# Performance work log

Hardware: AMD Instinct MI355X
Metric: run time of the kernel (lower is better)

## Reference

```python
import jax, jax.numpy as jnp
import numpy as np

EPS = 1e-7


def _softsplat(ten_in, ten_flow):
    # Forward bilinear splatting (scatter-add), faithful to softsplat_func.
    # ten_in: [B,C,H,W], ten_flow: [B,2,H,W] (flow[:,0]=dx, flow[:,1]=dy)
    B, C, H, W = ten_in.shape
    dt = ten_in.dtype
    gx = jnp.arange(W, dtype=dt)
    gy = jnp.arange(H, dtype=dt)
    fx = gx[None, None, :] + ten_flow[:, 0]  # [B,H,W] target x
    fy = gy[None, :, None] + ten_flow[:, 1]  # [B,H,W] target y
    x0 = jnp.floor(fx)
    y0 = jnp.floor(fy)
    x0i = x0.astype(jnp.int32)
    y0i = y0.astype(jnp.int32)
    x1i = x0i + 1
    y1i = y0i + 1
    wx1 = fx - x0  # weight toward x1
    wx0 = 1.0 - wx1
    wy1 = fy - y0
    wy0 = 1.0 - wy1
    # values as [B*H*W, C] rows to scatter
    vals = jnp.transpose(ten_in, (0, 2, 3, 1)).reshape(B * H * W, C)
    boff = jnp.arange(B, dtype=jnp.int32)[:, None, None] * (H * W)  # batch offsets
    out = jnp.zeros((B * H * W, C), dtype=dt)
    corners = ((x0i, y0i, wx0 * wy0), (x1i, y0i, wx1 * wy0),
               (x0i, y1i, wx0 * wy1), (x1i, y1i, wx1 * wy1))
    for xi, yi, w in corners:
        valid = (xi >= 0) & (xi < W) & (yi >= 0) & (yi < H)
        idx = (boff + jnp.clip(yi, 0, H - 1) * W + jnp.clip(xi, 0, W - 1)).reshape(-1)
        wv = jnp.where(valid, w, jnp.zeros_like(w)).reshape(-1, 1)
        out = out.at[idx].add(vals * wv)
    return jnp.transpose(out.reshape(B, H, W, C), (0, 3, 1, 2))


def reference(ten_in, ten_flow, ten_metric):
    # warp(..., strMode='soft'): softmax-style splatting with exp(metric) weights
    m = jnp.exp(ten_metric)                       # [B,1,H,W]
    cat = jnp.concatenate([ten_in * m, m], axis=1)  # [B,C+1,H,W]
    out = _softsplat(cat, ten_flow)
    norm = out[:, -1:, :, :] + EPS                # 'addeps' default branch
    return out[:, :-1, :, :] / norm


def setup_inputs() -> dict:
    key = jax.random.key(0)
    k1, k2, k3 = jax.random.split(key, 3)
    B, C, H, W = 4, 16, 512, 960
    ten_in = jax.random.normal(k1, (B, C, H, W), dtype=jnp.float32)
    # scale flow so splatting is genuinely irregular (multi-pixel displacements)
    ten_flow = jax.random.normal(k2, (B, 2, H, W), dtype=jnp.float32) * 10.0
    ten_metric = jax.random.normal(k3, (B, 1, H, W), dtype=jnp.float32)
    return {"ten_in": ten_in, "ten_flow": ten_flow, "ten_metric": ten_metric}
```

## Files before the change

### kernel.cpp

```cpp
#include <hip/hip_runtime.h>
#include <math.h>


#define BB 4
#define CC 16
#define HH 512
#define WW 960
#define HWP (HH * WW)
#define EPSF 1e-7f

#define NSX 30
#define NSY 256
#define SPB (NSX * NSY)
#define CAPS 192

#define WS_BINS_OFF ((size_t)131072)
#define WS_INT_OFF  (WS_BINS_OFF + (size_t)BB * SPB * CAPS * 16)
#define WS_NEED6    (WS_INT_OFF + (size_t)BB * HWP * 64)

#define TSX 32
#define TSY 16
#define TNX (WW / TSX)
#define TNY (HH / TSY)
#define TPB (TNX * TNY)
#define NTILE (BB * TPB)
#define CAP 1536


__launch_bounds__(256)
__global__ void prep6(const float* __restrict__ in,
                      const float* __restrict__ flow,
                      const float* __restrict__ metric,
                      unsigned int* __restrict__ counts,
                      uint4* __restrict__ bins,
                      float4* __restrict__ inT)
{
    __shared__ unsigned int lcnt[SPB];

    int b = blockIdx.z;
    int x = blockIdx.x * 32 + (threadIdx.x & 31);
    int y = blockIdx.y * 8  + (threadIdx.x >> 5);
    int p = y * WW + x;

    unsigned int* cb = counts + (size_t)b * SPB;
    uint4*        bb = bins   + (size_t)b * SPB * CAPS;

    for (int i = threadIdx.x; i < SPB; i += 256) lcnt[i] = 0;
    __syncthreads();

    float dx = flow[(size_t)(b * 2 + 0) * HWP + p];
    float dy = flow[(size_t)(b * 2 + 1) * HWP + p];
    float m  = expf(metric[(size_t)b * HWP + p]);

    const float* ib = in + (size_t)b * CC * HWP + p;
    float4* o = inT + ((size_t)b * HWP + p) * 4;
#pragma unroll
    for (int k = 0; k < 4; ++k) {
        float4 r;
        r.x = ib[(size_t)(4 * k + 0) * HWP];
        r.y = ib[(size_t)(4 * k + 1) * HWP];
        r.z = ib[(size_t)(4 * k + 2) * HWP];
        r.w = ib[(size_t)(4 * k + 3) * HWP];
        o[k] = r;
    }

    float fx = (float)x + dx, fy = (float)y + dy;
    float x0f = floorf(fx),   y0f = floorf(fy);
    int   x0 = (int)x0f,      y0 = (int)y0f;
    float wx1 = fx - x0f,     wy1 = fy - y0f;
    float wy0m = (1.0f - wy1) * m, wy1m = wy1 * m;

    int sxA = x0 >> 5, sxB = (x0 + 1) >> 5;
    int syA = y0 >> 1, syB = (y0 + 1) >> 1;
    bool dupX = (sxB != sxA);
    bool dupY = (syB != syA);

    float w0AB = dupY ? 0.0f  : wy0m;
    float w1AB = dupY ? wy0m  : wy1m;
    float w0CD = wy1m;

    bool vA = (sxA >= 0 && sxA < NSX && syA >= 0 && syA < NSY);
    bool vB = dupX && (sxB >= 0 && sxB < NSX && syA >= 0 && syA < NSY);
    bool vC = dupY && (sxA >= 0 && sxA < NSX && syB >= 0 && syB < NSY);
    bool vD = dupX && dupY && (sxB >= 0 && sxB < NSX && syB >= 0 && syB < NSY);

    int tA = syA * NSX + sxA, tB = syA * NSX + sxB;
    int tC = syB * NSX + sxA, tD = syB * NSX + sxB;

    unsigned int rA = 0, rB = 0, rC = 0, rD = 0;
    if (vA) rA = atomicAdd(&lcnt[tA], 1u);
    if (vB) rB = atomicAdd(&lcnt[tB], 1u);
    if (vC) rC = atomicAdd(&lcnt[tC], 1u);
    if (vD) rD = atomicAdd(&lcnt[tD], 1u);

    __syncthreads();

    for (int i = threadIdx.x; i < SPB; i += 256) {
        unsigned int c = lcnt[i];
        if (c) lcnt[i] = atomicAdd(&cb[i], c);
    }
    __syncthreads();

    unsigned int pkA = (unsigned int)p | ((unsigned int)((x0 - (sxA << 5)) + 1) << 19);
    unsigned int pkB = (unsigned int)p;
    unsigned int uwx = __float_as_uint(wx1);

    if (vA) { unsigned int pos = lcnt[tA] + rA;
        if (pos < CAPS) bb[(size_t)tA * CAPS + pos] =
            make_uint4(pkA, uwx, __float_as_uint(w0AB), __float_as_uint(w1AB)); }
    if (vB) { unsigned int pos = lcnt[tB] + rB;
        if (pos < CAPS) bb[(size_t)tB * CAPS + pos] =
            make_uint4(pkB, uwx, __float_as_uint(w0AB), __float_as_uint(w1AB)); }
    if (vC) { unsigned int pos = lcnt[tC] + rC;
        if (pos < CAPS) bb[(size_t)tC * CAPS + pos] =
            make_uint4(pkA, uwx, __float_as_uint(w0CD), __float_as_uint(0.0f)); }
    if (vD) { unsigned int pos = lcnt[tD] + rD;
        if (pos < CAPS) bb[(size_t)tD * CAPS + pos] =
            make_uint4(pkB, uwx, __float_as_uint(w0CD), __float_as_uint(0.0f)); }
}

__launch_bounds__(256)
__global__ void splat6(const float4* __restrict__ inT,
                       const unsigned int* __restrict__ counts,
                       const uint4* __restrict__ bins,
                       float* __restrict__ out)
{
    int wave = threadIdx.x >> 6;
    int lane = threadIdx.x & 63;
    int b    = blockIdx.z;
    int bx   = blockIdx.x;
    int sy   = blockIdx.y * 4 + wave;
    int s = __builtin_amdgcn_readfirstlane(sy * NSX + bx);

    unsigned int n = counts[(size_t)b * SPB + s];
    if (n > CAPS) n = CAPS;
    const uint4*  bs  = bins + ((size_t)b * SPB + s) * CAPS;
    const float4* ibT = inT + (size_t)b * HWP * 4;

    int lx = lane & 31;
    int ly = lane >> 5;

    float4 A = make_float4(0.f,0.f,0.f,0.f), B = A, C = A, D = A;
    float  aw = 0.f;

    #define LOADE(idx) (((unsigned int)(idx) < n) ? bs[idx] \
                                                  : make_uint4(0u,0u,0u,0u))

    #define DOFMA(eK, t0, t1, t2, t3)                                          \
        {                                                                      \
            int   cx  = (int)((eK.x >> 19) & 63u) - 1;                         \
            float wx1 = __uint_as_float(eK.y);                                 \
            float wrm = __uint_as_float(ly ? eK.w : eK.z);                     \
            float wx  = (lx == cx) ? (1.0f - wx1)                              \
                      : ((lx == cx + 1) ? wx1 : 0.0f);                         \
            float w   = wx * wrm;                                              \
            A.x += w*t0.x; A.y += w*t0.y; A.z += w*t0.z; A.w += w*t0.w;        \
            B.x += w*t1.x; B.y += w*t1.y; B.z += w*t1.z; B.w += w*t1.w;        \
            C.x += w*t2.x; C.y += w*t2.y; C.z += w*t2.z; C.w += w*t2.w;        \
            D.x += w*t3.x; D.y += w*t3.y; D.z += w*t3.z; D.w += w*t3.w;        \
            aw  += w;                                                          \
        }

    uint4 e0 = LOADE(0), e1 = LOADE(1);
    for (unsigned int j = 0; j < n; j += 2) {
        const float4* r0 = ibT + (size_t)(e0.x & 0x7FFFFu) * 4;
        const float4* r1 = ibT + (size_t)(e1.x & 0x7FFFFu) * 4;
        float4 t00 = r0[0], t01 = r0[1], t02 = r0[2], t03 = r0[3];
        float4 t10 = r1[0], t11 = r1[1], t12 = r1[2], t13 = r1[3];
        uint4 f0 = LOADE(j + 2), f1 = LOADE(j + 3);
        DOFMA(e0, t00, t01, t02, t03)
        DOFMA(e1, t10, t11, t12, t13)
        e0 = f0; e1 = f1;
    }
    #undef DOFMA
    #undef LOADE

    float inv = 1.0f / (aw + EPSF);
    int xg = bx * 32 + lx;
    int yg = sy * 2 + ly;
    float* ob = out + (size_t)b * CC * HWP + (size_t)yg * WW + xg;
    ob[(size_t) 0 * HWP] = A.x * inv;  ob[(size_t) 1 * HWP] = A.y * inv;
    ob[(size_t) 2 * HWP] = A.z * inv;  ob[(size_t) 3 * HWP] = A.w * inv;
    ob[(size_t) 4 * HWP] = B.x * inv;  ob[(size_t) 5 * HWP] = B.y * inv;
    ob[(size_t) 6 * HWP] = B.z * inv;  ob[(size_t) 7 * HWP] = B.w * inv;
    ob[(size_t) 8 * HWP] = C.x * inv;  ob[(size_t) 9 * HWP] = C.y * inv;
    ob[(size_t)10 * HWP] = C.z * inv;  ob[(size_t)11 * HWP] = C.w * inv;
    ob[(size_t)12 * HWP] = D.x * inv;  ob[(size_t)13 * HWP] = D.y * inv;
    ob[(size_t)14 * HWP] = D.z * inv;  ob[(size_t)15 * HWP] = D.w * inv;
}


__launch_bounds__(256)
__global__ void bin_kernel(const float* __restrict__ flow,
                           unsigned int* __restrict__ counts,
                           unsigned int* __restrict__ bins)
{
    __shared__ unsigned int lcnt[TPB];

    int b  = blockIdx.z;
    int x  = blockIdx.x * 32 + (threadIdx.x & 31);
    int y  = blockIdx.y * 8  + (threadIdx.x >> 5);
    int p  = y * WW + x;

    for (int i = threadIdx.x; i < TPB; i += 256) lcnt[i] = 0;
    __syncthreads();

    float dx = flow[(size_t)(b * 2 + 0) * HWP + p];
    float dy = flow[(size_t)(b * 2 + 1) * HWP + p];
    int x0 = (int)floorf((float)x + dx);
    int y0 = (int)floorf((float)y + dy);

    int txA = x0 >> 5, txB = (x0 + 1) >> 5;
    int tyA = y0 >> 4, tyB = (y0 + 1) >> 4;

    int          tA[4];
    unsigned int rA[4];
    int cnt = 0;

    #define TRYINS(tx_, ty_)                                                   \
        if ((tx_) >= 0 && (tx_) < TNX && (ty_) >= 0 && (ty_) < TNY) {          \
            int t_ = (ty_) * TNX + (tx_);                                      \
            rA[cnt] = atomicAdd(&lcnt[t_], 1u);                                \
            tA[cnt] = t_;                                                      \
            ++cnt;                                                             \
        }

    TRYINS(txA, tyA);
    if (txB != txA) TRYINS(txB, tyA);
    if (tyB != tyA) {
        TRYINS(txA, tyB);
        if (txB != txA) TRYINS(txB, tyB);
    }
    #undef TRYINS

    __syncthreads();

    for (int i = threadIdx.x; i < TPB; i += 256) {
        unsigned int c = lcnt[i];
        if (c) lcnt[i] = atomicAdd(&counts[b * TPB + i], c);
    }
    __syncthreads();

    unsigned int e = ((unsigned int)y << 10) | (unsigned int)x;
    for (int k = 0; k < cnt; ++k) {
        int t_ = tA[k];
        unsigned int pos = lcnt[t_] + rA[k];
        if (pos < CAP)
            bins[((size_t)(b * TPB) + t_) * CAP + pos] = e;
    }
}

__launch_bounds__(256)
__global__ void tile_kernel(const float* __restrict__ in,
                            const float* __restrict__ flow,
                            const float* __restrict__ metric,
                            const unsigned int* __restrict__ counts,
                            const unsigned int* __restrict__ bins,
                            float* __restrict__ out)
{
    __shared__ float acc[TSX * TSY * 17];

    int tile = blockIdx.x;
    int b  = tile / TPB;
    int t  = tile - b * TPB;
    int ty = t / TNX;
    int tx = t - ty * TNX;
    int tid = threadIdx.x;

    for (int i = tid; i < TSX * TSY * 17; i += 256) acc[i] = 0.0f;
    __syncthreads();

    unsigned int n = counts[tile];
    if (n > CAP) n = CAP;

    for (unsigned int base = 0; base < n; base += 256) {
        unsigned int i = base + tid;
        if (i < n) {
            unsigned int e = bins[(size_t)tile * CAP + i];
            int x = (int)(e & 1023u);
            int y = (int)(e >> 10);
            int p = y * WW + x;

            float dx = flow[(size_t)(b * 2 + 0) * HWP + p];
            float dy = flow[(size_t)(b * 2 + 1) * HWP + p];
            float m  = expf(metric[(size_t)b * HWP + p]);

            float fx = (float)x + dx;
            float fy = (float)y + dy;
            float x0f = floorf(fx), y0f = floorf(fy);
            int   x0  = (int)x0f,   y0  = (int)y0f;
            float wx1 = fx - x0f,   wy1 = fy - y0f;
            float wx0 = 1.0f - wx1, wy0 = 1.0f - wy1;

            float v[CC];
            const float* inp = in + (size_t)b * CC * HWP + p;
#pragma unroll
            for (int c = 0; c < CC; ++c) v[c] = inp[(size_t)c * HWP] * m;

            const int   xs[4] = { x0,        x0 + 1,    x0,        x0 + 1    };
            const int   ys[4] = { y0,        y0,        y0 + 1,    y0 + 1    };
            const float ws[4] = { wx0 * wy0, wx1 * wy0, wx0 * wy1, wx1 * wy1 };

#pragma unroll
            for (int k = 0; k < 4; ++k) {
                int xi = xs[k], yi = ys[k];
                if ((xi >> 5) == tx && (yi >> 4) == ty) {
                    float wgt = ws[k];
                    int q = ((yi & 15) * TSX + (xi & 31)) * 17;
#pragma unroll
                    for (int c = 0; c < CC; ++c)
                        atomicAdd(&acc[q + c], v[c] * wgt);
                    atomicAdd(&acc[q + CC], m * wgt);
                }
            }
        }
    }
    __syncthreads();

    for (int q = tid; q < TSX * TSY; q += 256) {
        int ly = q >> 5, lx = q & 31;
        int gp = (ty * TSY + ly) * WW + tx * TSX + lx;
        float inv = 1.0f / (acc[q * 17 + CC] + EPSF);
        float* op = out + (size_t)b * CC * HWP + gp;
#pragma unroll
        for (int c = 0; c < CC; ++c)
            op[(size_t)c * HWP] = acc[q * 17 + c] * inv;
    }
}


extern "C" void kernel_launch(void* const* d_in, const int* in_sizes, int n_in,
                              void* d_out, int out_size, void* d_ws, size_t ws_size,
                              hipStream_t stream) {
    const float* in     = (const float*)d_in[0];
    const float* flow   = (const float*)d_in[1];
    const float* metric = (const float*)d_in[2];
    float* out = (float*)d_out;

    if (ws_size >= WS_NEED6) {
        unsigned int* counts = (unsigned int*)d_ws;
        uint4*        bins   = (uint4*)((char*)d_ws + WS_BINS_OFF);
        float4*       inT    = (float4*)((char*)d_ws + WS_INT_OFF);

        hipMemsetAsync(counts, 0, (size_t)BB * SPB * 4, stream);

        prep6 <<<dim3(NSX, 64, BB), dim3(256), 0, stream>>>(
            in, flow, metric, counts, bins, inT);
        splat6<<<dim3(NSX, 64, BB), dim3(256), 0, stream>>>(
            inT, counts, bins, out);
    } else {
        unsigned int* counts = (unsigned int*)d_ws;
        unsigned int* bins   = (unsigned int*)((char*)d_ws + 16384);

        hipMemsetAsync(counts, 0, NTILE * sizeof(unsigned int), stream);

        bin_kernel<<<dim3(WW / 32, HH / 8, BB), dim3(256), 0, stream>>>(flow, counts, bins);
        tile_kernel<<<dim3(NTILE), dim3(256), 0, stream>>>(in, flow, metric, counts, bins, out);
    }
}
```

Baseline: 508.9 us.

## Split transpose into vectorized kernel and deepen splat gather prefetch pipeline

Moves the channel transpose out of the binning kernel into a separate kernel that reads float4 columns per channel and writes four pixels' rows per thread. The splat loop now prefetches the input rows two entries ahead and bin entries four ahead, loading out-of-range entries from a zeroed workspace slot instead of using a select. Together these aim to hide gather latency and widen memory accesses, at the cost of an extra kernel launch, higher register pressure, and scalar bin indexing being changed to per-lane vector indexing.

Result: slower. 787.6 us (+54.7%).

```diff
diff --git a/kernel.cpp b/kernel.cpp
--- a/kernel.cpp
+++ b/kernel.cpp
@@ -14,9 +14,10 @@
 #define SPB (NSX * NSY)
 #define CAPS 192
 
+#define WS_ZERO_OFF ((size_t)(BB * SPB * 4))
 #define WS_BINS_OFF ((size_t)131072)
 #define WS_INT_OFF  (WS_BINS_OFF + (size_t)BB * SPB * CAPS * 16)
-#define WS_NEED6    (WS_INT_OFF + (size_t)BB * HWP * 64)
+#define WS_NEED7    (WS_INT_OFF + (size_t)BB * HWP * 64)
 
 #define TSX 32
 #define TSY 16
@@ -28,12 +29,10 @@
 
 
 __launch_bounds__(256)
-__global__ void prep6(const float* __restrict__ in,
-                      const float* __restrict__ flow,
-                      const float* __restrict__ metric,
-                      unsigned int* __restrict__ counts,
-                      uint4* __restrict__ bins,
-                      float4* __restrict__ inT)
+__global__ void bin7(const float* __restrict__ flow,
+                     const float* __restrict__ metric,
+                     unsigned int* __restrict__ counts,
+                     uint4* __restrict__ bins)
 {
     __shared__ unsigned int lcnt[SPB];
 
@@ -51,18 +50,6 @@
     float dx = flow[(size_t)(b * 2 + 0) * HWP + p];
     float dy = flow[(size_t)(b * 2 + 1) * HWP + p];
     float m  = expf(metric[(size_t)b * HWP + p]);
-
-    const float* ib = in + (size_t)b * CC * HWP + p;
-    float4* o = inT + ((size_t)b * HWP + p) * 4;
-#pragma unroll
-    for (int k = 0; k < 4; ++k) {
-        float4 r;
-        r.x = ib[(size_t)(4 * k + 0) * HWP];
-        r.y = ib[(size_t)(4 * k + 1) * HWP];
-        r.z = ib[(size_t)(4 * k + 2) * HWP];
-        r.w = ib[(size_t)(4 * k + 3) * HWP];
-        o[k] = r;
-    }
 
     float fx = (float)x + dx, fy = (float)y + dy;
     float x0f = floorf(fx),   y0f = floorf(fy);
@@ -120,9 +107,53 @@
 }
 
 __launch_bounds__(256)
-__global__ void splat6(const float4* __restrict__ inT,
+__global__ void trans7(const float* __restrict__ in,
+                       float4* __restrict__ inT)
+{
+    int b = blockIdx.z;
+    int q = blockIdx.x * 256 + threadIdx.x;
+    int p = q * 4;
+
+    const float* ib = in + (size_t)b * CC * HWP + p;
+    float4* o = inT + ((size_t)b * HWP + p) * 4;
+
+    float4 col[16];
+#pragma unroll
+    for (int c = 0; c < CC; ++c)
+        col[c] = *(const float4*)(ib + (size_t)c * HWP);
+
+    #define WPX(px, COMP)                                                        \
+        o[(px)*4+0] = make_float4(col[ 0].COMP, col[ 1].COMP, col[ 2].COMP, col[ 3].COMP); \
+        o[(px)*4+1] = make_float4(col[ 4].COMP, col[ 5].COMP, col[ 6].COMP, col[ 7].COMP); \
+        o[(px)*4+2] = make_float4(col[ 8].COMP, col[ 9].COMP, col[10].COMP, col[11].COMP); \
+        o[(px)*4+3] = make_float4(col[12].COMP, col[13].COMP, col[14].COMP, col[15].COMP);
+    WPX(0, x) WPX(1, y) WPX(2, z) WPX(3, w)
+    #undef WPX
+}
+
+__device__ __forceinline__ uint4 lde7(const uint4* __restrict__ bs,
+                                      unsigned int j, unsigned int n,
+                                      const uint4* __restrict__ zp)
+{
+    unsigned int jj = j;
+    asm("" : "+v"(jj));
+    const uint4* a = (jj < n) ? (bs + jj) : zp;
+    return *a;
+}
+
+__device__ __forceinline__ const float4* rowp7(const float4* __restrict__ ibT,
+                                               unsigned int ex)
+{
+    unsigned int pv = ex & 0x7FFFFu;
+    asm("" : "+v"(pv));
+    return ibT + (size_t)pv * 4;
+}
+
+__launch_bounds__(256)
+__global__ void splat7(const float4* __restrict__ inT,
                        const unsigned int* __restrict__ counts,
                        const uint4* __restrict__ bins,
+                       const uint4* __restrict__ zp,
                        float* __restrict__ out)
 {
     int wave = threadIdx.x >> 6;
@@ -130,7 +161,7 @@
     int b    = blockIdx.z;
     int bx   = blockIdx.x;
     int sy   = blockIdx.y * 4 + wave;
-    int s = __builtin_amdgcn_readfirstlane(sy * NSX + bx);
+    int s    = sy * NSX + bx;
 
     unsigned int n = counts[(size_t)b * SPB + s];
     if (n > CAPS) n = CAPS;
@@ -142,9 +173,6 @@
 
     float4 A = make_float4(0.f,0.f,0.f,0.f), B = A, C = A, D = A;
     float  aw = 0.f;
-
-    #define LOADE(idx) (((unsigned int)(idx) < n) ? bs[idx] \
-                                                  : make_uint4(0u,0u,0u,0u))
 
     #define DOFMA(eK, t0, t1, t2, t3)                                          \
         {                                                                      \
@@ -161,19 +189,24 @@
             aw  += w;                                                          \
         }
 
-    uint4 e0 = LOADE(0), e1 = LOADE(1);
+    uint4 e0 = lde7(bs, 0, n, zp), e1 = lde7(bs, 1, n, zp);
+    const float4* rp;
+    rp = rowp7(ibT, e0.x); float4 R00=rp[0], R01=rp[1], R02=rp[2], R03=rp[3];
+    rp = rowp7(ibT, e1.x); float4 R10=rp[0], R11=rp[1], R12=rp[2], R13=rp[3];
+    uint4 e2 = lde7(bs, 2, n, zp), e3 = lde7(bs, 3, n, zp);
+
+#pragma unroll 2
     for (unsigned int j = 0; j < n; j += 2) {
-        const float4* r0 = ibT + (size_t)(e0.x & 0x7FFFFu) * 4;
-        const float4* r1 = ibT + (size_t)(e1.x & 0x7FFFFu) * 4;
-        float4 t00 = r0[0], t01 = r0[1], t02 = r0[2], t03 = r0[3];
-        float4 t10 = r1[0], t11 = r1[1], t12 = r1[2], t13 = r1[3];
-        uint4 f0 = LOADE(j + 2), f1 = LOADE(j + 3);
-        DOFMA(e0, t00, t01, t02, t03)
-        DOFMA(e1, t10, t11, t12, t13)
-        e0 = f0; e1 = f1;
+        uint4 f0 = lde7(bs, j + 4, n, zp), f1 = lde7(bs, j + 5, n, zp);
+        rp = rowp7(ibT, e2.x); float4 S00=rp[0], S01=rp[1], S02=rp[2], S03=rp[3];
+        rp = rowp7(ibT, e3.x); float4 S10=rp[0], S11=rp[1], S12=rp[2], S13=rp[3];
+        DOFMA(e0, R00, R01, R02, R03)
+        DOFMA(e1, R10, R11, R12, R13)
+        e0 = e2; e1 = e3; e2 = f0; e3 = f1;
+        R00=S00; R01=S01; R02=S02; R03=S03;
+        R10=S10; R11=S11; R12=S12; R13=S13;
     }
     #undef DOFMA
-    #undef LOADE
 
     float inv = 1.0f / (aw + EPSF);
     int xg = bx * 32 + lx;
@@ -337,17 +370,19 @@
     const float* metric = (const float*)d_in[2];
     float* out = (float*)d_out;
 
-    if (ws_size >= WS_NEED6) {
+    if (ws_size >= WS_NEED7) {
         unsigned int* counts = (unsigned int*)d_ws;
+        const uint4*  zp     = (const uint4*)((char*)d_ws + WS_ZERO_OFF);
         uint4*        bins   = (uint4*)((char*)d_ws + WS_BINS_OFF);
         float4*       inT    = (float4*)((char*)d_ws + WS_INT_OFF);
 
-        hipMemsetAsync(counts, 0, (size_t)BB * SPB * 4, stream);
-
-        prep6 <<<dim3(NSX, 64, BB), dim3(256), 0, stream>>>(
-            in, flow, metric, counts, bins, inT);
-        splat6<<<dim3(NSX, 64, BB), dim3(256), 0, stream>>>(
-            inT, counts, bins, out);
+        hipMemsetAsync(d_ws, 0, WS_ZERO_OFF + 16, stream);
+
+        bin7  <<<dim3(NSX, 64, BB),        dim3(256), 0, stream>>>(
+            flow, metric, counts, bins);
+        trans7<<<dim3(HWP / 4 / 256, 1, BB), dim3(256), 0, stream>>>(in, inT);
+        splat7<<<dim3(NSX, 64, BB),        dim3(256), 0, stream>>>(
+            inT, counts, bins, zp, out);
     } else {
         unsigned int* counts = (unsigned int*)d_ws;
         unsigned int* bins   = (unsigned int*)((char*)d_ws + 16384);
```
